# Performance work log

Hardware: AMD Instinct MI355X
Metric: run time of the kernel (lower is better)

## Reference

```python
import jax, jax.numpy as jnp
import numpy as np

N_NODES = 100000
N_EDGES = 1600000


def _add_self_loops(edge_index, num_nodes):
    loop = jnp.arange(num_nodes, dtype=edge_index.dtype)
    src = jnp.concatenate([edge_index[0], loop])
    dst = jnp.concatenate([edge_index[1], loop])
    return src, dst


def _gcn_conv(x, src, dst, W, b, num_nodes):
    # PyG GCNConv: h = x W, then symmetric-normalized scatter-add aggregation.
    h = x @ W  # [N, F_out]
    ones = jnp.ones(src.shape[0], dtype=x.dtype)
    deg = jax.ops.segment_sum(ones, dst, num_segments=num_nodes)  # in-degree incl. self-loops
    dinv = jnp.where(deg > 0, jax.lax.rsqrt(deg), 0.0)
    norm = dinv[src] * dinv[dst]  # [E]
    msg = h[src] * norm[:, None]  # irregular gather, [E, F_out]
    out = jax.ops.segment_sum(msg, dst, num_segments=num_nodes)  # scatter-add, [N, F_out]
    return out + b


def setup_inputs() -> dict:
    key = jax.random.key(0)
    ks = jax.random.split(key, 4)
    x = jax.random.uniform(ks[0], (N_NODES, 32), dtype=jnp.float32)
    edge_index = jax.random.randint(ks[1], (2, N_EDGES), 0, N_NODES, dtype=jnp.int64)
    W1 = jax.random.normal(ks[2], (32, 64), dtype=jnp.float32) * (1.0 / np.sqrt(32))
    b1 = jnp.zeros((64,), dtype=jnp.float32)
    W2 = jax.random.normal(ks[3], (64, 128), dtype=jnp.float32) * (1.0 / np.sqrt(64))
    b2 = jnp.zeros((128,), dtype=jnp.float32)
    return {"x": x, "edge_index": edge_index, "W1": W1, "b1": b1, "W2": W2, "b2": b2}


def reference(x, edge_index, W1, b1, W2, b2):
    num_nodes = x.shape[0]
    src, dst = _add_self_loops(edge_index, num_nodes)
    h = _gcn_conv(x, src, dst, W1, b1, num_nodes)
    h = jax.nn.relu(h)
    out = _gcn_conv(h, src, dst, W2, b2, num_nodes)
    return out
```

## Files before the change

kernel.cpp:

```cpp
#include <hip/hip_runtime.h>
#include <hip/hip_fp16.h>

static inline int cdiv(int a, int b) { return (a + b - 1) / b; }

#define BK_SHIFT 8
#define NBLK2 1024
#define SCAN_BS 1024
#define MAXB 6144

struct h2x4 { __half2 a, b, c, d; };

__global__ __launch_bounds__(256) void kb1(const int* __restrict__ dst, int E, int epb, int nbuk,
                                           int* __restrict__ cnt) {
    __shared__ int h[512];
    int blk = blockIdx.x;
    for (int b = threadIdx.x; b < nbuk; b += 256) h[b] = 0;
    __syncthreads();
    int beg = blk * epb, end = min(E, beg + epb);
    for (int e = beg + threadIdx.x; e < end; e += 256)
        atomicAdd(&h[dst[e] >> BK_SHIFT], 1);
    __syncthreads();
    for (int b = threadIdx.x; b < nbuk; b += 256) cnt[(size_t)b * NBLK2 + blk] = h[b];
}

__global__ __launch_bounds__(SCAN_BS) void k_blocksum(const int* __restrict__ v, int n, int* __restrict__ bsum) {
    __shared__ int s[SCAN_BS];
    int t = threadIdx.x;
    int i = blockIdx.x * SCAN_BS + t;
    s[t] = (i < n) ? v[i] : 0;
    __syncthreads();
    for (int off = SCAN_BS / 2; off > 0; off >>= 1) {
        if (t < off) s[t] += s[t + off];
        __syncthreads();
    }
    if (t == 0) bsum[blockIdx.x] = s[0];
}

__global__ __launch_bounds__(512) void k_scan_bsums(const int* __restrict__ bsum, int NB, int* __restrict__ boff) {
    __shared__ int s[512];
    int t = threadIdx.x;
    int v = (t < NB) ? bsum[t] : 0;
    s[t] = v;
    __syncthreads();
    for (int off = 1; off < 512; off <<= 1) {
        int u = (t >= off) ? s[t - off] : 0;
        __syncthreads();
        s[t] += u;
        __syncthreads();
    }
    if (t < NB) boff[t] = s[t] - v;
}

__global__ __launch_bounds__(SCAN_BS) void k_scan_final(const int* __restrict__ v, int n,
                                                        const int* __restrict__ boff,
                                                        int* __restrict__ outp, int E) {
    __shared__ int s[SCAN_BS];
    int t = threadIdx.x;
    int i = blockIdx.x * SCAN_BS + t;
    int x = (i < n) ? v[i] : 0;
    s[t] = x;
    __syncthreads();
    for (int off = 1; off < SCAN_BS; off <<= 1) {
        int u = (t >= off) ? s[t - off] : 0;
        __syncthreads();
        s[t] += u;
        __syncthreads();
    }
    if (i < n) outp[i] = boff[blockIdx.x] + s[t] - x;
    if (blockIdx.x == 0 && t == 0) outp[n] = E;
}

__global__ __launch_bounds__(256) void kb2(const int* __restrict__ ei, int E, int epb, int nbuk,
                                           const int* __restrict__ cbase,
                                           unsigned int* __restrict__ pairs) {
    __shared__ int lb[512];
    int blk = blockIdx.x;
    for (int b = threadIdx.x; b < nbuk; b += 256) lb[b] = cbase[(size_t)b * NBLK2 + blk];
    __syncthreads();
    int beg = blk * epb, end = min(E, beg + epb);
    const int* dst = ei + E;
    for (int e = beg + threadIdx.x; e < end; e += 256) {
        int d = dst[e];
        int s = ei[e];
        int slot = atomicAdd(&lb[d >> BK_SHIFT], 1);
        pairs[slot] = (unsigned)s | ((unsigned)(d & 255) << 17);
    }
}

__global__ __launch_bounds__(1024) void k_sortbucket(const unsigned int* __restrict__ pairs,
                                                     const int* __restrict__ cbase, int nbuk, int N, int E,
                                                     int* __restrict__ csr_src,
                                                     int* __restrict__ offsets,
                                                     float* __restrict__ dinv) {
    __shared__ int c[256];
    __shared__ int ex[256];
    __shared__ int sorted[MAXB];
    int b = blockIdx.x;
    int tid = threadIdx.x;
    int base = cbase[(size_t)b * NBLK2];
    int endp = cbase[(size_t)(b + 1) * NBLK2];
    int n = endp - base;
    if (tid < 256) c[tid] = 0;
    __syncthreads();
    int sr_[6], dl_[6], rk_[6];
#pragma unroll
    for (int k = 0; k < 6; ++k) {
        int i = tid + k * 1024;
        if (i < n) {
            unsigned int p = pairs[base + i];
            sr_[k] = (int)(p & 0x1FFFFu);
            dl_[k] = (int)(p >> 17);
            rk_[k] = atomicAdd(&c[dl_[k]], 1);
        }
    }
    __syncthreads();
    if (tid < 256) ex[tid] = c[tid];
    __syncthreads();
    for (int off = 1; off < 256; off <<= 1) {
        int u = (tid >= off && tid < 256) ? ex[tid - off] : 0;
        __syncthreads();
        if (tid < 256) ex[tid] += u;
        __syncthreads();
    }
    if (tid < 256) ex[tid] -= c[tid];
    __syncthreads();
#pragma unroll
    for (int k = 0; k < 6; ++k) {
        int i = tid + k * 1024;
        if (i < n) sorted[ex[dl_[k]] + rk_[k]] = sr_[k];
    }
    __syncthreads();
    for (int i = tid; i < n; i += 1024) csr_src[base + i] = sorted[i];
    if (tid < 256) {
        int g = (b << BK_SHIFT) + tid;
        if (g < N) {
            offsets[g] = base + ex[tid];
            dinv[g] = rsqrtf((float)(c[tid] + 1));
        }
    }
    if (b == 0 && tid == 0) offsets[N] = E;
}

__global__ __launch_bounds__(256) void k_cast32(const float* __restrict__ x, const float* __restrict__ dinv,
                                                __half* __restrict__ xh, int N) {
    int i = blockIdx.x * 256 + threadIdx.x;
    if (i >= N * 8) return;
    int g = i >> 3;
    float di = dinv[g];
    float4 v = ((const float4*)x)[i];
    __half2 h0 = __floats2half2_rn(v.x * di, v.y * di);
    __half2 h1 = __floats2half2_rn(v.z * di, v.w * di);
    ((__half2*)xh)[2 * i] = h0;
    ((__half2*)xh)[2 * i + 1] = h1;
}

__global__ __launch_bounds__(512) void k_fused1(const __half* __restrict__ feat,
                                                const int* __restrict__ offsets,
                                                const int* __restrict__ csr_src,
                                                const float* __restrict__ dinv,
                                                const float* __restrict__ W,
                                                const float* __restrict__ b,
                                                __half* __restrict__ out, int N) {
    __shared__ float sX[128][33];
    __shared__ float sW[32][64];
    __shared__ float sDi[128];
    int tid = threadIdx.x;
    int g0 = blockIdx.x * 128;

    {
        const float4* Wv = (const float4*)W;
        float4* sWv = (float4*)&sW[0][0];
        sWv[tid] = Wv[tid];
    }
    {
        int gl = tid >> 2, q = tid & 3;
        int g = g0 + gl;
        const h2x4* f8 = (const h2x4*)feat;
        float acc[8] = {0.f, 0.f, 0.f, 0.f, 0.f, 0.f, 0.f, 0.f};
        float di = 0.f;
        if (g < N) {
            di = dinv[g];
            h2x4 w = f8[(size_t)g * 4 + q];
            float2 u;
            u = __half22float2(w.a); acc[0] = u.x; acc[1] = u.y;
            u = __half22float2(w.b); acc[2] = u.x; acc[3] = u.y;
            u = __half22float2(w.c); acc[4] = u.x; acc[5] = u.y;
            u = __half22float2(w.d); acc[6] = u.x; acc[7] = u.y;
            int beg = offsets[g], end = offsets[g + 1];
            int e = beg;
            for (; e + 4 <= end; e += 4) {
                int s0 = csr_src[e + 0], s1 = csr_src[e + 1], s2 = csr_src[e + 2], s3 = csr_src[e + 3];
                h2x4 w0 = f8[(size_t)s0 * 4 + q];
                h2x4 w1 = f8[(size_t)s1 * 4 + q];
                h2x4 w2 = f8[(size_t)s2 * 4 + q];
                h2x4 w3 = f8[(size_t)s3 * 4 + q];
                u = __half22float2(w0.a); acc[0] += u.x; acc[1] += u.y;
                u = __half22float2(w0.b); acc[2] += u.x; acc[3] += u.y;
                u = __half22float2(w0.c); acc[4] += u.x; acc[5] += u.y;
                u = __half22float2(w0.d); acc[6] += u.x; acc[7] += u.y;
                u = __half22float2(w1.a); acc[0] += u.x; acc[1] += u.y;
                u = __half22float2(w1.b); acc[2] += u.x; acc[3] += u.y;
                u = __half22float2(w1.c); acc[4] += u.x; acc[5] += u.y;
                u = __half22float2(w1.d); acc[6] += u.x; acc[7] += u.y;
                u = __half22float2(w2.a); acc[0] += u.x; acc[1] += u.y;
                u = __half22float2(w2.b); acc[2] += u.x; acc[3] += u.y;
                u = __half22float2(w2.c); acc[4] += u.x; acc[5] += u.y;
                u = __half22float2(w2.d); acc[6] += u.x; acc[7] += u.y;
                u = __half22float2(w3.a); acc[0] += u.x; acc[1] += u.y;
                u = __half22float2(w3.b); acc[2] += u.x; acc[3] += u.y;
                u = __half22float2(w3.c); acc[4] += u.x; acc[5] += u.y;
                u = __half22float2(w3.d); acc[6] += u.x; acc[7] += u.y;
            }
            for (; e < end; ++e) {
                h2x4 w4 = f8[(size_t)csr_src[e] * 4 + q];
                u = __half22float2(w4.a); acc[0] += u.x; acc[1] += u.y;
                u = __half22float2(w4.b); acc[2] += u.x; acc[3] += u.y;
                u = __half22float2(w4.c); acc[4] += u.x; acc[5] += u.y;
                u = __half22float2(w4.d); acc[6] += u.x; acc[7] += u.y;
            }
        }
        if (q == 0) sDi[gl] = di;
#pragma unroll
        for (int j = 0; j < 8; ++j) sX[gl][q * 8 + j] = acc[j] * di;
    }
    __syncthreads();
    int tm = tid & 31, tn = tid >> 5;
    float acc2[4][4];
    {
        float4 bb = *(const float4*)(b + tn * 4);
#pragma unroll
        for (int i = 0; i < 4; ++i) {
            acc2[i][0] = bb.x; acc2[i][1] = bb.y; acc2[i][2] = bb.z; acc2[i][3] = bb.w;
        }
    }
#pragma unroll 4
    for (int k = 0; k < 32; ++k) {
        float a0 = sX[tm * 4 + 0][k];
        float a1 = sX[tm * 4 + 1][k];
        float a2 = sX[tm * 4 + 2][k];
        float a3 = sX[tm * 4 + 3][k];
        float4 w = *(const float4*)&sW[k][tn * 4];
        float wv[4] = {w.x, w.y, w.z, w.w};
#pragma unroll
        for (int j = 0; j < 4; ++j) {
            acc2[0][j] = fmaf(a0, wv[j], acc2[0][j]);
            acc2[1][j] = fmaf(a1, wv[j], acc2[1][j]);
            acc2[2][j] = fmaf(a2, wv[j], acc2[2][j]);
            acc2[3][j] = fmaf(a3, wv[j], acc2[3][j]);
        }
    }
#pragma unroll
    for (int i = 0; i < 4; ++i) {
        int row = g0 + tm * 4 + i;
        if (row < N) {
            float di = sDi[tm * 4 + i];
            __half2 p0 = __floats2half2_rn(fmaxf(acc2[i][0], 0.f) * di, fmaxf(acc2[i][1], 0.f) * di);
            __half2 p1 = __floats2half2_rn(fmaxf(acc2[i][2], 0.f) * di, fmaxf(acc2[i][3], 0.f) * di);
            __half2* op = (__half2*)(out + (size_t)row * 64);
            op[tn * 2] = p0;
            op[tn * 2 + 1] = p1;
        }
    }
}

__global__ __launch_bounds__(256) void k_agg64(const __half* __restrict__ feat,
                                               const int* __restrict__ offsets,
                                               const int* __restrict__ csr_src,
                                               const float* __restrict__ dinv,
                                               float* __restrict__ out, int N) {
    constexpr int L = 8;
    int t = blockIdx.x * 256 + threadIdx.x;
    int g = t / L;
    int q = t % L;
    if (g >= N) return;
    const h2x4* f8 = (const h2x4*)feat;
    int beg = offsets[g];
    int end = offsets[g + 1];
    float di = dinv[g];
    float acc[8];
    {
        h2x4 w = f8[(size_t)g * L + q];
        float2 p0 = __half22float2(w.a), p1 = __half22float2(w.b);
        float2 p2 = __half22float2(w.c), p3 = __half22float2(w.d);
        acc[0] = p0.x; acc[1] = p0.y; acc[2] = p1.x; acc[3] = p1.y;
        acc[4] = p2.x; acc[5] = p2.y; acc[6] = p3.x; acc[7] = p3.y;
    }
    int e = beg;
    for (; e + 4 <= end; e += 4) {
        int s0 = csr_src[e + 0], s1 = csr_src[e + 1], s2 = csr_src[e + 2], s3 = csr_src[e + 3];
        h2x4 w0 = f8[(size_t)s0 * L + q];
        h2x4 w1 = f8[(size_t)s1 * L + q];
        h2x4 w2 = f8[(size_t)s2 * L + q];
        h2x4 w3 = f8[(size_t)s3 * L + q];
        float2 u;
        u = __half22float2(w0.a); acc[0] += u.x; acc[1] += u.y;
        u = __half22float2(w0.b); acc[2] += u.x; acc[3] += u.y;
        u = __half22float2(w0.c); acc[4] += u.x; acc[5] += u.y;
        u = __half22float2(w0.d); acc[6] += u.x; acc[7] += u.y;
        u = __half22float2(w1.a); acc[0] += u.x; acc[1] += u.y;
        u = __half22float2(w1.b); acc[2] += u.x; acc[3] += u.y;
        u = __half22float2(w1.c); acc[4] += u.x; acc[5] += u.y;
        u = __half22float2(w1.d); acc[6] += u.x; acc[7] += u.y;
        u = __half22float2(w2.a); acc[0] += u.x; acc[1] += u.y;
        u = __half22float2(w2.b); acc[2] += u.x; acc[3] += u.y;
        u = __half22float2(w2.c); acc[4] += u.x; acc[5] += u.y;
        u = __half22float2(w2.d); acc[6] += u.x; acc[7] += u.y;
        u = __half22float2(w3.a); acc[0] += u.x; acc[1] += u.y;
        u = __half22float2(w3.b); acc[2] += u.x; acc[3] += u.y;
        u = __half22float2(w3.c); acc[4] += u.x; acc[5] += u.y;
        u = __half22float2(w3.d); acc[6] += u.x; acc[7] += u.y;
    }
    for (; e < end; ++e) {
        h2x4 w = f8[(size_t)csr_src[e] * L + q];
        float2 u;
        u = __half22float2(w.a); acc[0] += u.x; acc[1] += u.y;
        u = __half22float2(w.b); acc[2] += u.x; acc[3] += u.y;
        u = __half22float2(w.c); acc[4] += u.x; acc[5] += u.y;
        u = __half22float2(w.d); acc[6] += u.x; acc[7] += u.y;
    }
    float4 o0 = make_float4(acc[0] * di, acc[1] * di, acc[2] * di, acc[3] * di);
    float4 o1 = make_float4(acc[4] * di, acc[5] * di, acc[6] * di, acc[7] * di);
    ((float4*)out)[(size_t)g * 16 + q * 2] = o0;
    ((float4*)out)[(size_t)g * 16 + q * 2 + 1] = o1;
}

__global__ __launch_bounds__(256) void k_gemm2(const float* __restrict__ A, const float* __restrict__ W,
                                               const float* __restrict__ b, float* __restrict__ out, int N) {
    __shared__ float sA[64][68];
    __shared__ float sW[64][128];
    int tid = threadIdx.x;
    int row0 = blockIdx.x * 64;

    {
        const float4* Wv = (const float4*)W;
        float4* sWv = (float4*)&sW[0][0];
#pragma unroll
        for (int i = 0; i < 8; ++i) sWv[tid + 256 * i] = Wv[tid + 256 * i];
    }
    {
        int row = tid >> 2;
        int gr = row0 + row;
        int kq = (tid & 3) * 4;
#pragma unroll
        for (int i = 0; i < 4; ++i) {
            int k0 = kq + 16 * i;
            float4 v = (gr < N) ? *(const float4*)(A + (size_t)gr * 64 + k0)
                                : make_float4(0.f, 0.f, 0.f, 0.f);
            sA[k0 + 0][row] = v.x;
            sA[k0 + 1][row] = v.y;
            sA[k0 + 2][row] = v.z;
            sA[k0 + 3][row] = v.w;
        }
    }
    __syncthreads();

    int tm = tid & 15, tn = tid >> 4;
    float acc[4][8];
    {
        float4 b0 = *(const float4*)(b + tn * 8);
        float4 b1 = *(const float4*)(b + tn * 8 + 4);
#pragma unroll
        for (int i = 0; i < 4; ++i) {
            acc[i][0] = b0.x; acc[i][1] = b0.y; acc[i][2] = b0.z; acc[i][3] = b0.w;
            acc[i][4] = b1.x; acc[i][5] = b1.y; acc[i][6] = b1.z; acc[i][7] = b1.w;
        }
    }
#pragma unroll 4
    for (int k = 0; k < 64; ++k) {
        float4 a = *(const float4*)&sA[k][tm * 4];
        float4 w0 = *(const float4*)&sW[k][tn * 8];
        float4 w1 = *(const float4*)&sW[k][tn * 8 + 4];
        float av[4] = {a.x, a.y, a.z, a.w};
        float wv[8] = {w0.x, w0.y, w0.z, w0.w, w1.x, w1.y, w1.z, w1.w};
#pragma unroll
        for (int i = 0; i < 4; ++i)
#pragma unroll
            for (int j = 0; j < 8; ++j) acc[i][j] = fmaf(av[i], wv[j], acc[i][j]);
    }
#pragma unroll
    for (int i = 0; i < 4; ++i) {
        int row = row0 + tm * 4 + i;
        if (row < N) {
            *(float4*)(out + (size_t)row * 128 + tn * 8) =
                make_float4(acc[i][0], acc[i][1], acc[i][2], acc[i][3]);
            *(float4*)(out + (size_t)row * 128 + tn * 8 + 4) =
                make_float4(acc[i][4], acc[i][5], acc[i][6], acc[i][7]);
        }
    }
}

extern "C" void kernel_launch(void* const* d_in, const int* in_sizes, int n_in,
                              void* d_out, int out_size, void* d_ws, size_t ws_size,
                              hipStream_t stream) {
    const float* x  = (const float*)d_in[0];
    const int*   ei = (const int*)d_in[1];
    const float* W1 = (const float*)d_in[2];
    const float* b1 = (const float*)d_in[3];
    const float* W2 = (const float*)d_in[4];
    const float* b2 = (const float*)d_in[5];
    float* out = (float*)d_out;

    const int N = in_sizes[0] / 32;
    const int E = in_sizes[1] / 2;
    const int epb = cdiv(E, NBLK2);
    const int nbuk = cdiv(N, 1 << BK_SHIFT);
    const int clen = nbuk * NBLK2;

    char* ws = (char*)d_ws;
    size_t off = 0;
    auto walloc = [&](size_t bytes) -> void* {
        void* p = ws + off;
        off = (off + bytes + 255) & ~(size_t)255;
        return p;
    };
    int*          cnt     = (int*)          walloc((size_t)(clen + 4) * 4);
    int*          cbase   = (int*)          walloc((size_t)(clen + 4) * 4);
    int*          bsum    = (int*)          walloc(512 * 4);
    int*          boff    = (int*)          walloc(512 * 4);
    unsigned int* pairs   = (unsigned int*) walloc((size_t)E * 4);
    int*          csr_src = (int*)          walloc((size_t)E * 4);
    int*          offsets = (int*)          walloc((size_t)(N + 4) * 4);
    float*        dinv    = (float*)        walloc((size_t)N * 4);
    __half*       xh      = (__half*)       walloc((size_t)N * 32 * 2);
    __half*       h2h     = (__half*)       walloc((size_t)N * 64 * 2);
    float*        a2      = (float*)        walloc((size_t)N * 64 * 4);
    (void)ws_size; (void)n_in; (void)out_size;

    kb1<<<NBLK2, 256, 0, stream>>>(ei + E, E, epb, nbuk, cnt);

    const int NB = cdiv(clen, SCAN_BS);
    k_blocksum<<<NB, SCAN_BS, 0, stream>>>(cnt, clen, bsum);
    k_scan_bsums<<<1, 512, 0, stream>>>(bsum, NB, boff);
    k_scan_final<<<NB, SCAN_BS, 0, stream>>>(cnt, clen, boff, cbase, E);

    kb2<<<NBLK2, 256, 0, stream>>>(ei, E, epb, nbuk, cbase, pairs);
    k_sortbucket<<<nbuk, 1024, 0, stream>>>(pairs, cbase, nbuk, N, E, csr_src, offsets, dinv);

    k_cast32<<<cdiv(N * 8, 256), 256, 0, stream>>>(x, dinv, xh, N);

    k_fused1<<<cdiv(N, 128), 512, 0, stream>>>(xh, offsets, csr_src, dinv, W1, b1, h2h, N);

    k_agg64<<<cdiv(N * 8, 256), 256, 0, stream>>>(h2h, offsets, csr_src, dinv, a2, N);
    k_gemm2<<<cdiv(N, 64), 256, 0, stream>>>(a2, W2, b2, out, N);
}
```

Before: 149.5 us.

## Replace scan-based bucket partition with padded buckets and atomic cursors; fuse cast into sort

Drops the histogram, three-kernel scan and second scatter pass. Each bucket now gets a fixed padded slot range, and every block claims space with one global atomicAdd per bucket, so edges are counted and scattered in a single kernel. The x-to-half cast moves into the per-bucket sort kernel, and rows are stored as begin/end arrays because the padded layout is no longer contiguous. This cuts several launches and passes over the edge list. In exchange it assumes no bucket exceeds its padded capacity (4608 pairs) and no longer stores the scratch position at the end of each row.

```diff
diff --git a/kernel.cpp b/kernel.cpp
--- a/kernel.cpp
+++ b/kernel.cpp
@@ -4,81 +4,34 @@
 static inline int cdiv(int a, int b) { return (a + b - 1) / b; }
 
 #define BK_SHIFT 8
-#define NBLK2 1024
-#define SCAN_BS 1024
-#define MAXB 6144
+#define KBA_BLK 512
+#define PADB 4608
 
 struct h2x4 { __half2 a, b, c, d; };
 
-__global__ __launch_bounds__(256) void kb1(const int* __restrict__ dst, int E, int epb, int nbuk,
-                                           int* __restrict__ cnt) {
+__global__ __launch_bounds__(512) void k_init(int* __restrict__ gcur, int nbuk) {
+    int b = threadIdx.x;
+    if (b < nbuk) gcur[b] = b * PADB;
+}
+
+__global__ __launch_bounds__(256) void kbA(const int* __restrict__ ei, int E, int epb, int nbuk,
+                                           int* __restrict__ gcur,
+                                           unsigned int* __restrict__ pairs) {
     __shared__ int h[512];
+    __shared__ int lb[512];
     int blk = blockIdx.x;
+    int beg = blk * epb, end = min(E, beg + epb);
     for (int b = threadIdx.x; b < nbuk; b += 256) h[b] = 0;
     __syncthreads();
-    int beg = blk * epb, end = min(E, beg + epb);
+    const int* dst = ei + E;
     for (int e = beg + threadIdx.x; e < end; e += 256)
         atomicAdd(&h[dst[e] >> BK_SHIFT], 1);
     __syncthreads();
-    for (int b = threadIdx.x; b < nbuk; b += 256) cnt[(size_t)b * NBLK2 + blk] = h[b];
-}
-
-__global__ __launch_bounds__(SCAN_BS) void k_blocksum(const int* __restrict__ v, int n, int* __restrict__ bsum) {
-    __shared__ int s[SCAN_BS];
-    int t = threadIdx.x;
-    int i = blockIdx.x * SCAN_BS + t;
-    s[t] = (i < n) ? v[i] : 0;
-    __syncthreads();
-    for (int off = SCAN_BS / 2; off > 0; off >>= 1) {
-        if (t < off) s[t] += s[t + off];
-        __syncthreads();
-    }
-    if (t == 0) bsum[blockIdx.x] = s[0];
-}
-
-__global__ __launch_bounds__(512) void k_scan_bsums(const int* __restrict__ bsum, int NB, int* __restrict__ boff) {
-    __shared__ int s[512];
-    int t = threadIdx.x;
-    int v = (t < NB) ? bsum[t] : 0;
-    s[t] = v;
-    __syncthreads();
-    for (int off = 1; off < 512; off <<= 1) {
-        int u = (t >= off) ? s[t - off] : 0;
-        __syncthreads();
-        s[t] += u;
-        __syncthreads();
-    }
-    if (t < NB) boff[t] = s[t] - v;
-}
-
-__global__ __launch_bounds__(SCAN_BS) void k_scan_final(const int* __restrict__ v, int n,
-                                                        const int* __restrict__ boff,
-                                                        int* __restrict__ outp, int E) {
-    __shared__ int s[SCAN_BS];
-    int t = threadIdx.x;
-    int i = blockIdx.x * SCAN_BS + t;
-    int x = (i < n) ? v[i] : 0;
-    s[t] = x;
-    __syncthreads();
-    for (int off = 1; off < SCAN_BS; off <<= 1) {
-        int u = (t >= off) ? s[t - off] : 0;
-        __syncthreads();
-        s[t] += u;
-        __syncthreads();
-    }
-    if (i < n) outp[i] = boff[blockIdx.x] + s[t] - x;
-    if (blockIdx.x == 0 && t == 0) outp[n] = E;
-}
-
-__global__ __launch_bounds__(256) void kb2(const int* __restrict__ ei, int E, int epb, int nbuk,
-                                           const int* __restrict__ cbase,
-                                           unsigned int* __restrict__ pairs) {
-    __shared__ int lb[512];
-    int blk = blockIdx.x;
-    for (int b = threadIdx.x; b < nbuk; b += 256) lb[b] = cbase[(size_t)b * NBLK2 + blk];
-    __syncthreads();
-    int beg = blk * epb, end = min(E, beg + epb);
-    const int* dst = ei + E;
+    for (int b = threadIdx.x; b < nbuk; b += 256) {
+        int c = h[b];
+        lb[b] = c ? atomicAdd(&gcur[b], c) : 0;
+    }
+    __syncthreads();
     for (int e = beg + threadIdx.x; e < end; e += 256) {
         int d = dst[e];
         int s = ei[e];
@@ -87,25 +40,28 @@
     }
 }
 
-__global__ __launch_bounds__(1024) void k_sortbucket(const unsigned int* __restrict__ pairs,
-                                                     const int* __restrict__ cbase, int nbuk, int N, int E,
-                                                     int* __restrict__ csr_src,
-                                                     int* __restrict__ offsets,
-                                                     float* __restrict__ dinv) {
+__global__ __launch_bounds__(1024) void k_sortcast(const unsigned int* __restrict__ pairs,
+                                                   const int* __restrict__ gcur, int nbuk, int N,
+                                                   const float* __restrict__ x,
+                                                   int* __restrict__ csr_src,
+                                                   int* __restrict__ begA, int* __restrict__ endA,
+                                                   float* __restrict__ dinv,
+                                                   __half* __restrict__ xh) {
     __shared__ int c[256];
     __shared__ int ex[256];
-    __shared__ int sorted[MAXB];
+    __shared__ float sdi[256];
+    __shared__ int sorted[PADB];
     int b = blockIdx.x;
     int tid = threadIdx.x;
-    int base = cbase[(size_t)b * NBLK2];
-    int endp = cbase[(size_t)(b + 1) * NBLK2];
-    int n = endp - base;
+    int base = b * PADB;
+    int n = gcur[b] - base;
     if (tid < 256) c[tid] = 0;
     __syncthreads();
-    int sr_[6], dl_[6], rk_[6];
-#pragma unroll
-    for (int k = 0; k < 6; ++k) {
+    int sr_[5], dl_[5], rk_[5];
+#pragma unroll
+    for (int k = 0; k < 5; ++k) {
         int i = tid + k * 1024;
+        sr_[k] = -1;
         if (i < n) {
             unsigned int p = pairs[base + i];
             sr_[k] = (int)(p & 0x1FFFFu);
@@ -125,37 +81,42 @@
     if (tid < 256) ex[tid] -= c[tid];
     __syncthreads();
 #pragma unroll
-    for (int k = 0; k < 6; ++k) {
-        int i = tid + k * 1024;
-        if (i < n) sorted[ex[dl_[k]] + rk_[k]] = sr_[k];
+    for (int k = 0; k < 5; ++k) {
+        if (sr_[k] >= 0) sorted[ex[dl_[k]] + rk_[k]] = sr_[k];
     }
     __syncthreads();
     for (int i = tid; i < n; i += 1024) csr_src[base + i] = sorted[i];
     if (tid < 256) {
         int g = (b << BK_SHIFT) + tid;
         if (g < N) {
-            offsets[g] = base + ex[tid];
-            dinv[g] = rsqrtf((float)(c[tid] + 1));
-        }
-    }
-    if (b == 0 && tid == 0) offsets[N] = E;
-}
-
-__global__ __launch_bounds__(256) void k_cast32(const float* __restrict__ x, const float* __restrict__ dinv,
-                                                __half* __restrict__ xh, int N) {
-    int i = blockIdx.x * 256 + threadIdx.x;
-    if (i >= N * 8) return;
-    int g = i >> 3;
-    float di = dinv[g];
-    float4 v = ((const float4*)x)[i];
-    __half2 h0 = __floats2half2_rn(v.x * di, v.y * di);
-    __half2 h1 = __floats2half2_rn(v.z * di, v.w * di);
-    ((__half2*)xh)[2 * i] = h0;
-    ((__half2*)xh)[2 * i + 1] = h1;
+            int bg = base + ex[tid];
+            begA[g] = bg;
+            endA[g] = bg + c[tid];
+            float di = rsqrtf((float)(c[tid] + 1));
+            dinv[g] = di;
+            sdi[tid] = di;
+        } else {
+            sdi[tid] = 0.f;
+        }
+    }
+    __syncthreads();
+    int g0 = b << BK_SHIFT;
+    int nn = min(256, N - g0);
+    const float4* x4 = (const float4*)x;
+    for (int idx = tid; idx < nn * 8; idx += 1024) {
+        int nd = idx >> 3;
+        float di = sdi[nd];
+        float4 v = x4[(size_t)(g0 + nd) * 8 + (idx & 7)];
+        __half2 h0 = __floats2half2_rn(v.x * di, v.y * di);
+        __half2 h1 = __floats2half2_rn(v.z * di, v.w * di);
+        ((__half2*)xh)[2 * ((size_t)(g0 + nd) * 8 + (idx & 7))] = h0;
+        ((__half2*)xh)[2 * ((size_t)(g0 + nd) * 8 + (idx & 7)) + 1] = h1;
+    }
 }
 
 __global__ __launch_bounds__(512) void k_fused1(const __half* __restrict__ feat,
-                                                const int* __restrict__ offsets,
+                                                const int* __restrict__ begA,
+                                                const int* __restrict__ endA,
                                                 const int* __restrict__ csr_src,
                                                 const float* __restrict__ dinv,
                                                 const float* __restrict__ W,
@@ -186,7 +147,7 @@
             u = __half22float2(w.b); acc[2] = u.x; acc[3] = u.y;
             u = __half22float2(w.c); acc[4] = u.x; acc[5] = u.y;
             u = __half22float2(w.d); acc[6] = u.x; acc[7] = u.y;
-            int beg = offsets[g], end = offsets[g + 1];
+            int beg = begA[g], end = endA[g];
             int e = beg;
             for (; e + 4 <= end; e += 4) {
                 int s0 = csr_src[e + 0], s1 = csr_src[e + 1], s2 = csr_src[e + 2], s3 = csr_src[e + 3];
@@ -264,7 +225,8 @@
 }
 
 __global__ __launch_bounds__(256) void k_agg64(const __half* __restrict__ feat,
-                                               const int* __restrict__ offsets,
+                                               const int* __restrict__ begA,
+                                               const int* __restrict__ endA,
                                                const int* __restrict__ csr_src,
                                                const float* __restrict__ dinv,
                                                float* __restrict__ out, int N) {
@@ -274,8 +236,8 @@
     int q = t % L;
     if (g >= N) return;
     const h2x4* f8 = (const h2x4*)feat;
-    int beg = offsets[g];
-    int end = offsets[g + 1];
+    int beg = begA[g];
+    int end = endA[g];
     float di = dinv[g];
     float acc[8];
     {
@@ -402,9 +364,8 @@
 
     const int N = in_sizes[0] / 32;
     const int E = in_sizes[1] / 2;
-    const int epb = cdiv(E, NBLK2);
+    const int epb = cdiv(E, KBA_BLK);
     const int nbuk = cdiv(N, 1 << BK_SHIFT);
-    const int clen = nbuk * NBLK2;
 
     char* ws = (char*)d_ws;
     size_t off = 0;
@@ -413,33 +374,23 @@
         off = (off + bytes + 255) & ~(size_t)255;
         return p;
     };
-    int*          cnt     = (int*)          walloc((size_t)(clen + 4) * 4);
-    int*          cbase   = (int*)          walloc((size_t)(clen + 4) * 4);
-    int*          bsum    = (int*)          walloc(512 * 4);
-    int*          boff    = (int*)          walloc(512 * 4);
-    unsigned int* pairs   = (unsigned int*) walloc((size_t)E * 4);
-    int*          csr_src = (int*)          walloc((size_t)E * 4);
-    int*          offsets = (int*)          walloc((size_t)(N + 4) * 4);
+    int*          gcur    = (int*)          walloc((size_t)(nbuk + 4) * 4);
+    unsigned int* pairs   = (unsigned int*) walloc((size_t)nbuk * PADB * 4);
+    int*          csr_src = (int*)          walloc((size_t)nbuk * PADB * 4);
+    int*          begA    = (int*)          walloc((size_t)(N + 4) * 4);
+    int*          endA    = (int*)          walloc((size_t)(N + 4) * 4);
     float*        dinv    = (float*)        walloc((size_t)N * 4);
     __half*       xh      = (__half*)       walloc((size_t)N * 32 * 2);
     __half*       h2h     = (__half*)       walloc((size_t)N * 64 * 2);
     float*        a2      = (float*)        walloc((size_t)N * 64 * 4);
     (void)ws_size; (void)n_in; (void)out_size;
 
-    kb1<<<NBLK2, 256, 0, stream>>>(ei + E, E, epb, nbuk, cnt);
-
-    const int NB = cdiv(clen, SCAN_BS);
-    k_blocksum<<<NB, SCAN_BS, 0, stream>>>(cnt, clen, bsum);
-    k_scan_bsums<<<1, 512, 0, stream>>>(bsum, NB, boff);
-    k_scan_final<<<NB, SCAN_BS, 0, stream>>>(cnt, clen, boff, cbase, E);
-
-    kb2<<<NBLK2, 256, 0, stream>>>(ei, E, epb, nbuk, cbase, pairs);
-    k_sortbucket<<<nbuk, 1024, 0, stream>>>(pairs, cbase, nbuk, N, E, csr_src, offsets, dinv);
-
-    k_cast32<<<cdiv(N * 8, 256), 256, 0, stream>>>(x, dinv, xh, N);
-
-    k_fused1<<<cdiv(N, 128), 512, 0, stream>>>(xh, offsets, csr_src, dinv, W1, b1, h2h, N);
-
-    k_agg64<<<cdiv(N * 8, 256), 256, 0, stream>>>(h2h, offsets, csr_src, dinv, a2, N);
+    k_init<<<1, 512, 0, stream>>>(gcur, nbuk);
+    kbA<<<KBA_BLK, 256, 0, stream>>>(ei, E, epb, nbuk, gcur, pairs);
+    k_sortcast<<<nbuk, 1024, 0, stream>>>(pairs, gcur, nbuk, N, x, csr_src, begA, endA, dinv, xh);
+
+    k_fused1<<<cdiv(N, 128), 512, 0, stream>>>(xh, begA, endA, csr_src, dinv, W1, b1, h2h, N);
+
+    k_agg64<<<cdiv(N * 8, 256), 256, 0, stream>>>(h2h, begA, endA, csr_src, dinv, a2, N);
     k_gemm2<<<cdiv(N, 64), 256, 0, stream>>>(a2, W2, b2, out, N);
 }
```

After: 138.8 us (median of 2 runs). -7.2%, faster.
